# Optimization experiments

Measured on AMD Instinct MI355X. Metric: run time of the kernel, lower is better.

The kernel has to match this reference:

```python
import jax, jax.numpy as jnp
import numpy as np

NPIX = 12288
NBUCKETS = 32
IN_DIM = 32
OUT_DIM = 128
LN_EPS = 1e-5


def setup_inputs() -> dict:
    key = jax.random.key(0)
    ks = jax.random.split(key, 8)
    N = 2000000
    nbatch = 4
    obs_features = jax.random.normal(ks[0], (N, IN_DIM), dtype=jnp.float32)
    batch_idx = jax.random.randint(ks[1], (N,), 0, nbatch, dtype=jnp.int64 if jax.config.jax_enable_x64 else jnp.int32).astype(jnp.int32)
    pix = jax.random.randint(ks[2], (N,), 0, NPIX).astype(jnp.int32)
    bucket_id = jax.random.randint(ks[3], (N,), 0, NBUCKETS).astype(jnp.int32)
    proj_in = NBUCKETS * IN_DIM + NBUCKETS  # 1056
    proj_out = 2 * OUT_DIM  # 256
    W1 = jax.random.normal(ks[4], (proj_in, proj_out), dtype=jnp.float32) / np.sqrt(proj_in)
    b1 = jnp.zeros((proj_out,), dtype=jnp.float32)
    ln_g = jnp.ones((proj_out,), dtype=jnp.float32)
    ln_b = jnp.zeros((proj_out,), dtype=jnp.float32)
    W2 = jax.random.normal(ks[5], (proj_out, OUT_DIM), dtype=jnp.float32) / np.sqrt(proj_out)
    b2 = jnp.zeros((OUT_DIM,), dtype=jnp.float32)
    return {"obs_features": obs_features, "batch_idx": batch_idx, "pix": pix,
            "bucket_id": bucket_id, "nbatch": nbatch,
            "W1": W1, "b1": b1, "ln_g": ln_g, "ln_b": ln_b, "W2": W2, "b2": b2}


def reference(obs_features, batch_idx, pix, bucket_id, nbatch, W1, b1, ln_g, ln_b, W2, b2):
    # Flatten (batch, pix, bucket) coords row-major, as in scatter_mean's strides.
    flat_idx = (batch_idx.astype(jnp.int32) * (NPIX * NBUCKETS)
                + pix.astype(jnp.int32) * NBUCKETS
                + bucket_id.astype(jnp.int32))
    grid_size = nbatch * NPIX * NBUCKETS
    # scatter-mean: segment sums and counts over the flat grid
    sums = jax.ops.segment_sum(obs_features, flat_idx, num_segments=grid_size)  # (G, C)
    counts = jax.ops.segment_sum(jnp.ones((obs_features.shape[0],), obs_features.dtype),
                                 flat_idx, num_segments=grid_size)  # (G,)
    present = counts > 0
    # NaN fill for empty cells followed by nan_to_num(0) == zero fill for empty cells
    mean = jnp.where(present[:, None], sums / jnp.maximum(counts, 1.0)[:, None], 0.0)
    aggregated = mean.reshape(nbatch, NPIX, NBUCKETS * IN_DIM)
    has_obs = present.reshape(nbatch, NPIX, NBUCKETS).astype(obs_features.dtype)
    mlp_in = jnp.concatenate([aggregated, has_obs], axis=-1)  # (B, npix, proj_in)
    h = mlp_in @ W1 + b1
    mu = jnp.mean(h, axis=-1, keepdims=True)
    var = jnp.mean(jnp.square(h - mu), axis=-1, keepdims=True)
    h = (h - mu) * jax.lax.rsqrt(var + LN_EPS) * ln_g + ln_b
    h = jax.nn.silu(h)
    return h @ W2 + b2  # (B, npix, out_dim)
```

## Files before the change

kernel.cpp:

```cpp
#include <hip/hip_runtime.h>
#include <cstddef>
#include <cstdint>
#include <cmath>

#define NPIX     12288
#define NBUCKETS 32
#define IN_DIM   32
#define PROJ_IN  1056
#define PROJ_OUT 256
#define OUT_DIM  128
#define LN_EPS   1e-5f
#define NBATCH   4

#define ROWS   (NBATCH * NPIX)
#define GCELLS (ROWS * NBUCKETS)

#define BM 64
#define BK 32

#define SCAN_CHUNK 2048
#define NBLK_SCAN  (GCELLS / SCAN_CHUNK)

__global__ __launch_bounds__(256)
void flat_hist_kernel(const int* __restrict__ bidx, const int* __restrict__ pix,
                      const int* __restrict__ bucket, int* __restrict__ flat,
                      int* __restrict__ cnt, int N)
{
    int p = blockIdx.x * 256 + threadIdx.x;
    if (p >= N) return;
    int f = bidx[p] * (NPIX * NBUCKETS) + pix[p] * NBUCKETS + bucket[p];
    flat[p] = f;
    atomicAdd(&cnt[f], 1);
}

__global__ __launch_bounds__(256)
void scan_reduce_kernel(const int* __restrict__ cnt, int* __restrict__ partials)
{
    __shared__ int wsum[4];
    const int b = blockIdx.x, t = threadIdx.x;
    const int4* src = reinterpret_cast<const int4*>(cnt + (size_t)b * SCAN_CHUNK);
    int4 v0 = src[t * 2], v1 = src[t * 2 + 1];
    int s = v0.x + v0.y + v0.z + v0.w + v1.x + v1.y + v1.z + v1.w;
#pragma unroll
    for (int off = 32; off; off >>= 1) s += __shfl_xor(s, off);
    if ((t & 63) == 0) wsum[t >> 6] = s;
    __syncthreads();
    if (t == 0) partials[b] = wsum[0] + wsum[1] + wsum[2] + wsum[3];
}

__global__ void scan_mid_kernel(int* __restrict__ partials)
{
    const int t = threadIdx.x;
    int v[12]; int s = 0;
#pragma unroll
    for (int i = 0; i < 12; ++i) { v[i] = partials[t * 12 + i]; s += v[i]; }
    int inc = s;
#pragma unroll
    for (int d = 1; d < 64; d <<= 1) { int o = __shfl_up(inc, d); if (t >= d) inc += o; }
    int base = inc - s;
#pragma unroll
    for (int i = 0; i < 12; ++i) { int x = v[i]; partials[t * 12 + i] = base; base += x; }
}

__global__ __launch_bounds__(256)
void scan_write_kernel(const int* __restrict__ partials,
                       int* __restrict__ offs, int* __restrict__ cursor)
{
    __shared__ int wbase[4];
    const int b = blockIdx.x, t = threadIdx.x;
    const int lane = t & 63, w = t >> 6;
    const int4* src = reinterpret_cast<const int4*>(cursor + (size_t)b * SCAN_CHUNK);
    int4 v0 = src[t * 2], v1 = src[t * 2 + 1];
    int a[8] = { v0.x, v0.y, v0.z, v0.w, v1.x, v1.y, v1.z, v1.w };
    int s = 0;
#pragma unroll
    for (int i = 0; i < 8; ++i) s += a[i];
    int inc = s;
#pragma unroll
    for (int d = 1; d < 64; d <<= 1) { int o = __shfl_up(inc, d); if (lane >= d) inc += o; }
    if (lane == 63) wbase[w] = inc;
    __syncthreads();
    int wb = 0;
    for (int i = 0; i < w; ++i) wb += wbase[i];
    int base = partials[b] + wb + (inc - s);
    const int idx0 = b * SCAN_CHUNK + t * 8;
#pragma unroll
    for (int i = 0; i < 8; ++i) { offs[idx0 + i] = base; cursor[idx0 + i] = base; base += a[i]; }
    if (b == (int)gridDim.x - 1 && t == 255) offs[GCELLS] = base;
}

__global__ __launch_bounds__(256)
void reorder_kernel(const int* __restrict__ flat, int* __restrict__ cursor,
                    int* __restrict__ order, int N)
{
    int p = blockIdx.x * 256 + threadIdx.x;
    if (p >= N) return;
    int f = flat[p];
    int slot = atomicAdd(&cursor[f], 1);
    order[slot] = p;
}

__global__ void zero_out_kernel(float* __restrict__ out, size_t n)
{
    size_t i = (size_t)blockIdx.x * blockDim.x + threadIdx.x;
    if (i < n) out[i] = 0.f;
}

__global__ __launch_bounds__(256, 3)
void fused_mlp_kernel(const float* __restrict__ feats,
                      const int*   __restrict__ order_g,
                      const int*   __restrict__ offs_g,
                      const float* __restrict__ W1,
                      const float* __restrict__ b1,
                      const float* __restrict__ ln_g,
                      const float* __restrict__ ln_b,
                      const float* __restrict__ W2,
                      const float* __restrict__ b2,
                      float* __restrict__ out)
{
    __shared__ __align__(16) float smem[8192 + 2048 + 2052];
    float* Bs   = smem;
    float* As   = smem + 8192;
    int*   offsT = reinterpret_cast<int*>(smem + 8192 + 2048);
    float* h_s  = smem;

    const int t    = threadIdx.x;
    const int row0 = blockIdx.x * BM;
    const int tr   = t >> 5;
    const int tc   = t & 31;
    const int m0   = tr * 8;
    const int c0   = tc * 8;

    {
        const int4* s4 = reinterpret_cast<const int4*>(offs_g + (size_t)row0 * NBUCKETS);
        int4* d4 = reinterpret_cast<int4*>(offsT);
        d4[t]       = s4[t];
        d4[t + 256] = s4[t + 256];
        if (t == 0) offsT[2048] = offs_g[(size_t)row0 * NBUCKETS + 2048];
    }
    __syncthreads();

    float acc[8][8];
#pragma unroll
    for (int i = 0; i < 8; ++i)
#pragma unroll
        for (int j = 0; j < 8; ++j) acc[i][j] = 0.f;

    const int ar = t >> 3;
    const int aq = t & 7;
    const float4* feats4 = reinterpret_cast<const float4*>(feats);

    for (int s = 0; s < 33; ++s) {
        {
            const float4* src = reinterpret_cast<const float4*>(W1 + (size_t)s * BK * PROJ_OUT);
            float4* dst = reinterpret_cast<float4*>(Bs);
#pragma unroll
            for (int i = 0; i < 8; ++i) dst[t + i * 256] = src[t + i * 256];
        }
        if (s < 32) {
#pragma unroll
            for (int h = 0; h < 2; ++h) {
                const int r = ar + h * 32;
                const int cell = r * NBUCKETS + s;
                const int start = offsT[cell], end = offsT[cell + 1];
                float4 a4 = make_float4(0.f, 0.f, 0.f, 0.f);
                for (int j = start; j < end; ++j) {
                    const int idx = order_g[j];
                    const float4 v = feats4[(size_t)idx * 8 + aq];
                    a4.x += v.x; a4.y += v.y; a4.z += v.z; a4.w += v.w;
                }
                const int cnt = end - start;
                const float inv = cnt ? 1.0f / (float)cnt : 0.f;
                As[(aq * 4 + 0) * 64 + r] = a4.x * inv;
                As[(aq * 4 + 1) * 64 + r] = a4.y * inv;
                As[(aq * 4 + 2) * 64 + r] = a4.z * inv;
                As[(aq * 4 + 3) * 64 + r] = a4.w * inv;
            }
        } else {
#pragma unroll
            for (int h = 0; h < 2; ++h) {
                const int r = ar + h * 32;
#pragma unroll
                for (int i = 0; i < 4; ++i) {
                    const int kk = aq * 4 + i;
                    As[kk * 64 + r] = (offsT[r * NBUCKETS + kk + 1] > offsT[r * NBUCKETS + kk]) ? 1.f : 0.f;
                }
            }
        }
        __syncthreads();

#pragma unroll 8
        for (int kk = 0; kk < BK; ++kk) {
            float a[8], b[8];
            *reinterpret_cast<float4*>(&a[0]) = *reinterpret_cast<const float4*>(&As[kk * 64 + m0]);
            *reinterpret_cast<float4*>(&a[4]) = *reinterpret_cast<const float4*>(&As[kk * 64 + m0 + 4]);
            *reinterpret_cast<float4*>(&b[0]) = *reinterpret_cast<const float4*>(&Bs[kk * 256 + c0]);
            *reinterpret_cast<float4*>(&b[4]) = *reinterpret_cast<const float4*>(&Bs[kk * 256 + c0 + 4]);
#pragma unroll
            for (int i = 0; i < 8; ++i)
#pragma unroll
                for (int j = 0; j < 8; ++j)
                    acc[i][j] = fmaf(a[i], b[j], acc[i][j]);
        }
        __syncthreads();
    }

    float b1v[8];
    *reinterpret_cast<float4*>(&b1v[0]) = *reinterpret_cast<const float4*>(&b1[c0]);
    *reinterpret_cast<float4*>(&b1v[4]) = *reinterpret_cast<const float4*>(&b1[c0 + 4]);

    const int lane = t & 63;
    const int wv   = t >> 6;
    const float g0 = ln_g[lane], g1 = ln_g[lane + 64], g2 = ln_g[lane + 128], g3 = ln_g[lane + 192];
    const float e0 = ln_b[lane], e1 = ln_b[lane + 64], e2 = ln_b[lane + 128], e3 = ln_b[lane + 192];

    for (int half = 0; half < 2; ++half) {
        __syncthreads();
        if ((tr >> 2) == half) {
            const int mb = m0 - half * 32;
#pragma unroll
            for (int i = 0; i < 8; ++i) {
                float4 w0 = make_float4(acc[i][0] + b1v[0], acc[i][1] + b1v[1],
                                        acc[i][2] + b1v[2], acc[i][3] + b1v[3]);
                float4 w1 = make_float4(acc[i][4] + b1v[4], acc[i][5] + b1v[5],
                                        acc[i][6] + b1v[6], acc[i][7] + b1v[7]);
                *reinterpret_cast<float4*>(&h_s[(mb + i) * 256 + c0])     = w0;
                *reinterpret_cast<float4*>(&h_s[(mb + i) * 256 + c0 + 4]) = w1;
            }
        }
        __syncthreads();

        for (int r = wv; r < 32; r += 4) {
            float v0 = h_s[r * 256 + lane];
            float v1 = h_s[r * 256 + lane + 64];
            float v2 = h_s[r * 256 + lane + 128];
            float v3 = h_s[r * 256 + lane + 192];
            float sum = v0 + v1 + v2 + v3;
            float sq  = fmaf(v0, v0, fmaf(v1, v1, fmaf(v2, v2, v3 * v3)));
#pragma unroll
            for (int off = 32; off > 0; off >>= 1) {
                sum += __shfl_xor(sum, off);
                sq  += __shfl_xor(sq, off);
            }
            const float mu  = sum * (1.0f / 256.0f);
            const float var = sq * (1.0f / 256.0f) - mu * mu;
            const float rs  = rsqrtf(var + LN_EPS);
            v0 = fmaf((v0 - mu) * rs, g0, e0);
            v1 = fmaf((v1 - mu) * rs, g1, e1);
            v2 = fmaf((v2 - mu) * rs, g2, e2);
            v3 = fmaf((v3 - mu) * rs, g3, e3);
            v0 = v0 / (1.f + expf(-v0));
            v1 = v1 / (1.f + expf(-v1));
            v2 = v2 / (1.f + expf(-v2));
            v3 = v3 / (1.f + expf(-v3));
            h_s[r * 256 + lane]       = v0;
            h_s[r * 256 + lane + 64]  = v1;
            h_s[r * 256 + lane + 128] = v2;
            h_s[r * 256 + lane + 192] = v3;
        }
        __syncthreads();

        {
            const int c  = t & 127;
            const int gg = t >> 7;
            float acc2[16];
#pragma unroll
            for (int i = 0; i < 16; ++i) acc2[i] = 0.f;
            for (int k = 0; k < 256; k += 4) {
                const float wa = W2[(k + 0) * 128 + c];
                const float wb = W2[(k + 1) * 128 + c];
                const float wc = W2[(k + 2) * 128 + c];
                const float wd = W2[(k + 3) * 128 + c];
#pragma unroll
                for (int i = 0; i < 16; ++i) {
                    const float4 h4 = *reinterpret_cast<const float4*>(&h_s[(gg * 16 + i) * 256 + k]);
                    acc2[i] = fmaf(h4.x, wa, acc2[i]);
                    acc2[i] = fmaf(h4.y, wb, acc2[i]);
                    acc2[i] = fmaf(h4.z, wc, acc2[i]);
                    acc2[i] = fmaf(h4.w, wd, acc2[i]);
                }
            }
            const float bias = b2[c];
#pragma unroll
            for (int i = 0; i < 16; ++i) {
                const int m = gg * 16 + i;
                out[(size_t)(row0 + half * 32 + m) * 128 + c] = acc2[i] + bias;
            }
        }
    }
}

extern "C" void kernel_launch(void* const* d_in, const int* in_sizes, int n_in,
                              void* d_out, int out_size, void* d_ws, size_t ws_size,
                              hipStream_t stream)
{
    const float* feats  = (const float*)d_in[0];
    const int*   bidx   = (const int*)d_in[1];
    const int*   pix    = (const int*)d_in[2];
    const int*   bucket = (const int*)d_in[3];
    const float* W1   = (const float*)d_in[5];
    const float* b1   = (const float*)d_in[6];
    const float* ln_g = (const float*)d_in[7];
    const float* ln_b = (const float*)d_in[8];
    const float* W2   = (const float*)d_in[9];
    const float* b2   = (const float*)d_in[10];
    float* out = (float*)d_out;

    const int N = in_sizes[1];

    int* flat     = (int*)d_ws;
    int* order    = flat + N;
    int* cursor   = order + N;
    int* offs     = cursor + GCELLS;
    int* partials = offs + GCELLS + 1;

    const size_t ws_needed = ((size_t)2 * N + 2 * GCELLS + 1 + NBLK_SCAN) * sizeof(int);
    if (ws_size < ws_needed) {
        size_t n = (size_t)out_size;
        zero_out_kernel<<<(unsigned)((n + 255) / 256), 256, 0, stream>>>(out, n);
        return;
    }

    hipMemsetAsync(cursor, 0, (size_t)GCELLS * sizeof(int), stream);

    const int pgrid = (N + 255) / 256;
    flat_hist_kernel<<<pgrid, 256, 0, stream>>>(bidx, pix, bucket, flat, cursor, N);
    scan_reduce_kernel<<<NBLK_SCAN, 256, 0, stream>>>(cursor, partials);
    scan_mid_kernel<<<1, 64, 0, stream>>>(partials);
    scan_write_kernel<<<NBLK_SCAN, 256, 0, stream>>>(partials, offs, cursor);
    reorder_kernel<<<pgrid, 256, 0, stream>>>(flat, cursor, order, N);

    fused_mlp_kernel<<<ROWS / BM, 256, 0, stream>>>(feats, order, offs, W1, b1,
                                                    ln_g, ln_b, W2, b2, out);
}
```

Baseline: 1.049 ms.

## Move fused MLP onto bf16x3 MFMA with pre-swizzled split weights

Rewrites the fused scatter-mean MLP kernel so both GEMMs use 16x16x32 bf16 MFMA instructions. It emulates fp32 precision with hi/lo bf16 splits (three products per tile). A new kernel pre-swizzles W1 and W2 into per-lane bf16 hi/lo records each call. LayerNorm and SiLU now run directly on the accumulator registers instead of passing through shared memory. The reorder pass drops its second atomic by recording each point's rank during the histogram, at the cost of an extra N-sized rank buffer and some precision loss from the bf16 splitting.

```diff
diff --git a/kernel.cpp b/kernel.cpp
--- a/kernel.cpp
+++ b/kernel.cpp
@@ -15,22 +15,68 @@
 #define ROWS   (NBATCH * NPIX)
 #define GCELLS (ROWS * NBUCKETS)
 
-#define BM 64
-#define BK 32
-
 #define SCAN_CHUNK 2048
 #define NBLK_SCAN  (GCELLS / SCAN_CHUNK)
 
+#define W1RECS (33 * 16 * 64)
+#define W2RECS (8 * 8 * 64)
+
+typedef __attribute__((ext_vector_type(8))) short bf16x8;
+typedef __attribute__((ext_vector_type(4))) float f32x4;
+
+__device__ inline unsigned bf16_rne_bits(float v) {
+    unsigned u = __float_as_uint(v);
+    return (u + 0x7FFFu + ((u >> 16) & 1u)) >> 16;
+}
+
+__global__ __launch_bounds__(256)
+void swz_kernel(const float* __restrict__ W1, const float* __restrict__ W2,
+                bf16x8* __restrict__ w1h, bf16x8* __restrict__ w1l,
+                bf16x8* __restrict__ w2h, bf16x8* __restrict__ w2l)
+{
+    const int T = blockIdx.x * 256 + threadIdx.x;
+    if (T < W1RECS) {
+        const int l = T & 63, n0 = (T >> 6) & 15, s = T >> 10;
+        const int col  = n0 * 16 + (l & 15);
+        const int krow = s * 32 + (l >> 4) * 8;
+        bf16x8 vh, vl;
+#pragma unroll
+        for (int j = 0; j < 8; ++j) {
+            const float v = W1[(size_t)(krow + j) * PROJ_OUT + col];
+            const unsigned hb = bf16_rne_bits(v);
+            const float hf = __uint_as_float(hb << 16);
+            const unsigned lb = bf16_rne_bits(v - hf);
+            vh[j] = (short)hb; vl[j] = (short)lb;
+        }
+        w1h[T] = vh; w1l[T] = vl;
+    } else if (T < W1RECS + W2RECS) {
+        const int T2 = T - W1RECS;
+        const int l = T2 & 63, n0 = (T2 >> 6) & 7, s2 = T2 >> 9;
+        const int col  = n0 * 16 + (l & 15);
+        const int krow = s2 * 32 + (l >> 4) * 8;
+        bf16x8 vh, vl;
+#pragma unroll
+        for (int j = 0; j < 8; ++j) {
+            const float v = W2[(size_t)(krow + j) * OUT_DIM + col];
+            const unsigned hb = bf16_rne_bits(v);
+            const float hf = __uint_as_float(hb << 16);
+            const unsigned lb = bf16_rne_bits(v - hf);
+            vh[j] = (short)hb; vl[j] = (short)lb;
+        }
+        w2h[T2] = vh; w2l[T2] = vl;
+    }
+}
+
 __global__ __launch_bounds__(256)
 void flat_hist_kernel(const int* __restrict__ bidx, const int* __restrict__ pix,
                       const int* __restrict__ bucket, int* __restrict__ flat,
-                      int* __restrict__ cnt, int N)
+                      int* __restrict__ rank, int* __restrict__ cnt, int N)
 {
     int p = blockIdx.x * 256 + threadIdx.x;
     if (p >= N) return;
     int f = bidx[p] * (NPIX * NBUCKETS) + pix[p] * NBUCKETS + bucket[p];
     flat[p] = f;
-    atomicAdd(&cnt[f], 1);
+    rank[p] = atomicAdd(&cnt[f], 1);
 }
 
 __global__ __launch_bounds__(256)
@@ -63,13 +109,13 @@
 }
 
 __global__ __launch_bounds__(256)
-void scan_write_kernel(const int* __restrict__ partials,
-                       int* __restrict__ offs, int* __restrict__ cursor)
+void scan_write_kernel(const int* __restrict__ partials, const int* __restrict__ cnt,
+                       int* __restrict__ offs)
 {
     __shared__ int wbase[4];
     const int b = blockIdx.x, t = threadIdx.x;
     const int lane = t & 63, w = t >> 6;
-    const int4* src = reinterpret_cast<const int4*>(cursor + (size_t)b * SCAN_CHUNK);
+    const int4* src = reinterpret_cast<const int4*>(cnt + (size_t)b * SCAN_CHUNK);
     int4 v0 = src[t * 2], v1 = src[t * 2 + 1];
     int a[8] = { v0.x, v0.y, v0.z, v0.w, v1.x, v1.y, v1.z, v1.w };
     int s = 0;
@@ -85,19 +131,17 @@
     int base = partials[b] + wb + (inc - s);
     const int idx0 = b * SCAN_CHUNK + t * 8;
 #pragma unroll
-    for (int i = 0; i < 8; ++i) { offs[idx0 + i] = base; cursor[idx0 + i] = base; base += a[i]; }
+    for (int i = 0; i < 8; ++i) { offs[idx0 + i] = base; base += a[i]; }
     if (b == (int)gridDim.x - 1 && t == 255) offs[GCELLS] = base;
 }
 
 __global__ __launch_bounds__(256)
-void reorder_kernel(const int* __restrict__ flat, int* __restrict__ cursor,
-                    int* __restrict__ order, int N)
+void reorder_kernel(const int* __restrict__ flat, const int* __restrict__ rank,
+                    const int* __restrict__ offs, int* __restrict__ order, int N)
 {
     int p = blockIdx.x * 256 + threadIdx.x;
     if (p >= N) return;
-    int f = flat[p];
-    int slot = atomicAdd(&cursor[f], 1);
-    order[slot] = p;
+    order[offs[flat[p]] + rank[p]] = p;
 }
 
 __global__ void zero_out_kernel(float* __restrict__ out, size_t n)
@@ -107,185 +151,177 @@
 }
 
 __global__ __launch_bounds__(256, 3)
-void fused_mlp_kernel(const float* __restrict__ feats,
-                      const int*   __restrict__ order_g,
-                      const int*   __restrict__ offs_g,
-                      const float* __restrict__ W1,
-                      const float* __restrict__ b1,
-                      const float* __restrict__ ln_g,
-                      const float* __restrict__ ln_b,
-                      const float* __restrict__ W2,
-                      const float* __restrict__ b2,
-                      float* __restrict__ out)
-{
-    __shared__ __align__(16) float smem[8192 + 2048 + 2052];
-    float* Bs   = smem;
-    float* As   = smem + 8192;
-    int*   offsT = reinterpret_cast<int*>(smem + 8192 + 2048);
-    float* h_s  = smem;
-
-    const int t    = threadIdx.x;
-    const int row0 = blockIdx.x * BM;
-    const int tr   = t >> 5;
-    const int tc   = t & 31;
-    const int m0   = tr * 8;
-    const int c0   = tc * 8;
-
-    {
-        const int4* s4 = reinterpret_cast<const int4*>(offs_g + (size_t)row0 * NBUCKETS);
-        int4* d4 = reinterpret_cast<int4*>(offsT);
-        d4[t]       = s4[t];
-        d4[t + 256] = s4[t + 256];
-        if (t == 0) offsT[2048] = offs_g[(size_t)row0 * NBUCKETS + 2048];
+void fused_mlp_mfma(const float* __restrict__ feats,
+                    const int*   __restrict__ order_g,
+                    const int*   __restrict__ offs_g,
+                    const bf16x8* __restrict__ w1h, const bf16x8* __restrict__ w1l,
+                    const bf16x8* __restrict__ w2h, const bf16x8* __restrict__ w2l,
+                    const float* __restrict__ b1,   const float* __restrict__ ln_g,
+                    const float* __restrict__ ln_b, const float* __restrict__ b2,
+                    float* __restrict__ out)
+{
+    __shared__ int offsT[64 * 33];
+    __shared__ __align__(16) short hfH[4][2048];
+    __shared__ __align__(16) short hfL[4][2048];
+
+    const int t  = threadIdx.x;
+    const int w  = t >> 6;
+    const int l  = t & 63;
+    const int g  = l >> 4;
+    const int li = l & 15;
+    const int row0 = blockIdx.x * 64;
+    const int rl = w * 16 + li;
+
+    for (int i = t; i < 64 * 33; i += 256) {
+        const int r = i / 33, b = i - r * 33;
+        offsT[i] = offs_g[(size_t)row0 * 32 + r * 32 + b];
     }
     __syncthreads();
 
-    float acc[8][8];
-#pragma unroll
-    for (int i = 0; i < 8; ++i)
-#pragma unroll
-        for (int j = 0; j < 8; ++j) acc[i][j] = 0.f;
-
-    const int ar = t >> 3;
-    const int aq = t & 7;
+    f32x4 acc[16];
+#pragma unroll
+    for (int n0 = 0; n0 < 16; ++n0) acc[n0] = (f32x4){0.f, 0.f, 0.f, 0.f};
+
     const float4* feats4 = reinterpret_cast<const float4*>(feats);
 
     for (int s = 0; s < 33; ++s) {
-        {
-            const float4* src = reinterpret_cast<const float4*>(W1 + (size_t)s * BK * PROJ_OUT);
-            float4* dst = reinterpret_cast<float4*>(Bs);
-#pragma unroll
-            for (int i = 0; i < 8; ++i) dst[t + i * 256] = src[t + i * 256];
-        }
+        float m[8];
         if (s < 32) {
-#pragma unroll
-            for (int h = 0; h < 2; ++h) {
-                const int r = ar + h * 32;
-                const int cell = r * NBUCKETS + s;
-                const int start = offsT[cell], end = offsT[cell + 1];
-                float4 a4 = make_float4(0.f, 0.f, 0.f, 0.f);
-                for (int j = start; j < end; ++j) {
-                    const int idx = order_g[j];
-                    const float4 v = feats4[(size_t)idx * 8 + aq];
-                    a4.x += v.x; a4.y += v.y; a4.z += v.z; a4.w += v.w;
-                }
-                const int cnt = end - start;
-                const float inv = cnt ? 1.0f / (float)cnt : 0.f;
-                As[(aq * 4 + 0) * 64 + r] = a4.x * inv;
-                As[(aq * 4 + 1) * 64 + r] = a4.y * inv;
-                As[(aq * 4 + 2) * 64 + r] = a4.z * inv;
-                As[(aq * 4 + 3) * 64 + r] = a4.w * inv;
-            }
+            const int start = offsT[rl * 33 + s];
+            const int end   = offsT[rl * 33 + s + 1];
+            float4 a0 = make_float4(0.f, 0.f, 0.f, 0.f);
+            float4 a1 = make_float4(0.f, 0.f, 0.f, 0.f);
+            for (int j2 = start; j2 < end; ++j2) {
+                const int idx = order_g[j2];
+                const float4 p0 = feats4[(size_t)idx * 8 + g * 2];
+                const float4 p1 = feats4[(size_t)idx * 8 + g * 2 + 1];
+                a0.x += p0.x; a0.y += p0.y; a0.z += p0.z; a0.w += p0.w;
+                a1.x += p1.x; a1.y += p1.y; a1.z += p1.z; a1.w += p1.w;
+            }
+            const float inv = (end > start) ? 1.f / (float)(end - start) : 0.f;
+            m[0] = a0.x * inv; m[1] = a0.y * inv; m[2] = a0.z * inv; m[3] = a0.w * inv;
+            m[4] = a1.x * inv; m[5] = a1.y * inv; m[6] = a1.z * inv; m[7] = a1.w * inv;
         } else {
 #pragma unroll
-            for (int h = 0; h < 2; ++h) {
-                const int r = ar + h * 32;
-#pragma unroll
-                for (int i = 0; i < 4; ++i) {
-                    const int kk = aq * 4 + i;
-                    As[kk * 64 + r] = (offsT[r * NBUCKETS + kk + 1] > offsT[r * NBUCKETS + kk]) ? 1.f : 0.f;
-                }
-            }
-        }
-        __syncthreads();
-
-#pragma unroll 8
-        for (int kk = 0; kk < BK; ++kk) {
-            float a[8], b[8];
-            *reinterpret_cast<float4*>(&a[0]) = *reinterpret_cast<const float4*>(&As[kk * 64 + m0]);
-            *reinterpret_cast<float4*>(&a[4]) = *reinterpret_cast<const float4*>(&As[kk * 64 + m0 + 4]);
-            *reinterpret_cast<float4*>(&b[0]) = *reinterpret_cast<const float4*>(&Bs[kk * 256 + c0]);
-            *reinterpret_cast<float4*>(&b[4]) = *reinterpret_cast<const float4*>(&Bs[kk * 256 + c0 + 4]);
-#pragma unroll
-            for (int i = 0; i < 8; ++i)
-#pragma unroll
-                for (int j = 0; j < 8; ++j)
-                    acc[i][j] = fmaf(a[i], b[j], acc[i][j]);
-        }
-        __syncthreads();
-    }
-
-    float b1v[8];
-    *reinterpret_cast<float4*>(&b1v[0]) = *reinterpret_cast<const float4*>(&b1[c0]);
-    *reinterpret_cast<float4*>(&b1v[4]) = *reinterpret_cast<const float4*>(&b1[c0 + 4]);
-
-    const int lane = t & 63;
-    const int wv   = t >> 6;
-    const float g0 = ln_g[lane], g1 = ln_g[lane + 64], g2 = ln_g[lane + 128], g3 = ln_g[lane + 192];
-    const float e0 = ln_b[lane], e1 = ln_b[lane + 64], e2 = ln_b[lane + 128], e3 = ln_b[lane + 192];
-
-    for (int half = 0; half < 2; ++half) {
-        __syncthreads();
-        if ((tr >> 2) == half) {
-            const int mb = m0 - half * 32;
-#pragma unroll
-            for (int i = 0; i < 8; ++i) {
-                float4 w0 = make_float4(acc[i][0] + b1v[0], acc[i][1] + b1v[1],
-                                        acc[i][2] + b1v[2], acc[i][3] + b1v[3]);
-                float4 w1 = make_float4(acc[i][4] + b1v[4], acc[i][5] + b1v[5],
-                                        acc[i][6] + b1v[6], acc[i][7] + b1v[7]);
-                *reinterpret_cast<float4*>(&h_s[(mb + i) * 256 + c0])     = w0;
-                *reinterpret_cast<float4*>(&h_s[(mb + i) * 256 + c0 + 4]) = w1;
-            }
-        }
-        __syncthreads();
-
-        for (int r = wv; r < 32; r += 4) {
-            float v0 = h_s[r * 256 + lane];
-            float v1 = h_s[r * 256 + lane + 64];
-            float v2 = h_s[r * 256 + lane + 128];
-            float v3 = h_s[r * 256 + lane + 192];
-            float sum = v0 + v1 + v2 + v3;
-            float sq  = fmaf(v0, v0, fmaf(v1, v1, fmaf(v2, v2, v3 * v3)));
-#pragma unroll
-            for (int off = 32; off > 0; off >>= 1) {
-                sum += __shfl_xor(sum, off);
-                sq  += __shfl_xor(sq, off);
-            }
-            const float mu  = sum * (1.0f / 256.0f);
-            const float var = sq * (1.0f / 256.0f) - mu * mu;
-            const float rs  = rsqrtf(var + LN_EPS);
-            v0 = fmaf((v0 - mu) * rs, g0, e0);
-            v1 = fmaf((v1 - mu) * rs, g1, e1);
-            v2 = fmaf((v2 - mu) * rs, g2, e2);
-            v3 = fmaf((v3 - mu) * rs, g3, e3);
-            v0 = v0 / (1.f + expf(-v0));
-            v1 = v1 / (1.f + expf(-v1));
-            v2 = v2 / (1.f + expf(-v2));
-            v3 = v3 / (1.f + expf(-v3));
-            h_s[r * 256 + lane]       = v0;
-            h_s[r * 256 + lane + 64]  = v1;
-            h_s[r * 256 + lane + 128] = v2;
-            h_s[r * 256 + lane + 192] = v3;
-        }
-        __syncthreads();
-
-        {
-            const int c  = t & 127;
-            const int gg = t >> 7;
-            float acc2[16];
-#pragma unroll
-            for (int i = 0; i < 16; ++i) acc2[i] = 0.f;
-            for (int k = 0; k < 256; k += 4) {
-                const float wa = W2[(k + 0) * 128 + c];
-                const float wb = W2[(k + 1) * 128 + c];
-                const float wc = W2[(k + 2) * 128 + c];
-                const float wd = W2[(k + 3) * 128 + c];
-#pragma unroll
-                for (int i = 0; i < 16; ++i) {
-                    const float4 h4 = *reinterpret_cast<const float4*>(&h_s[(gg * 16 + i) * 256 + k]);
-                    acc2[i] = fmaf(h4.x, wa, acc2[i]);
-                    acc2[i] = fmaf(h4.y, wb, acc2[i]);
-                    acc2[i] = fmaf(h4.z, wc, acc2[i]);
-                    acc2[i] = fmaf(h4.w, wd, acc2[i]);
-                }
-            }
-            const float bias = b2[c];
-#pragma unroll
-            for (int i = 0; i < 16; ++i) {
-                const int m = gg * 16 + i;
-                out[(size_t)(row0 + half * 32 + m) * 128 + c] = acc2[i] + bias;
-            }
+            for (int j = 0; j < 8; ++j) {
+                const int b = g * 8 + j;
+                m[j] = (offsT[rl * 33 + b + 1] > offsT[rl * 33 + b]) ? 1.f : 0.f;
+            }
+        }
+        bf16x8 ah, al;
+#pragma unroll
+        for (int j = 0; j < 8; ++j) {
+            const unsigned u = __float_as_uint(m[j]);
+            ah[j] = (short)(u >> 16);
+            const float rlo = m[j] - __uint_as_float(u & 0xFFFF0000u);
+            al[j] = (short)(__float_as_uint(rlo) >> 16);
+        }
+        const int base = (s * 16) * 64 + l;
+        if (s < 32) {
+#pragma unroll 4
+            for (int n0 = 0; n0 < 16; ++n0) {
+                const bf16x8 bh = w1h[base + n0 * 64];
+                const bf16x8 bl = w1l[base + n0 * 64];
+                acc[n0] = __builtin_amdgcn_mfma_f32_16x16x32_bf16(ah, bh, acc[n0], 0, 0, 0);
+                acc[n0] = __builtin_amdgcn_mfma_f32_16x16x32_bf16(ah, bl, acc[n0], 0, 0, 0);
+                acc[n0] = __builtin_amdgcn_mfma_f32_16x16x32_bf16(al, bh, acc[n0], 0, 0, 0);
+            }
+        } else {
+#pragma unroll 4
+            for (int n0 = 0; n0 < 16; ++n0) {
+                const bf16x8 bh = w1h[base + n0 * 64];
+                const bf16x8 bl = w1l[base + n0 * 64];
+                acc[n0] = __builtin_amdgcn_mfma_f32_16x16x32_bf16(ah, bh, acc[n0], 0, 0, 0);
+                acc[n0] = __builtin_amdgcn_mfma_f32_16x16x32_bf16(ah, bl, acc[n0], 0, 0, 0);
+            }
+        }
+    }
+
+    float sum[4] = {0.f, 0.f, 0.f, 0.f}, sq[4] = {0.f, 0.f, 0.f, 0.f};
+#pragma unroll
+    for (int n0 = 0; n0 < 16; ++n0) {
+        const float bb = b1[n0 * 16 + li];
+#pragma unroll
+        for (int r = 0; r < 4; ++r) {
+            const float v = acc[n0][r] + bb;
+            acc[n0][r] = v;
+            sum[r] += v;
+            sq[r] = fmaf(v, v, sq[r]);
+        }
+    }
+#pragma unroll
+    for (int off = 1; off < 16; off <<= 1) {
+#pragma unroll
+        for (int r = 0; r < 4; ++r) {
+            sum[r] += __shfl_xor(sum[r], off);
+            sq[r]  += __shfl_xor(sq[r], off);
+        }
+    }
+    float mu[4], rs[4];
+#pragma unroll
+    for (int r = 0; r < 4; ++r) {
+        mu[r] = sum[r] * (1.f / 256.f);
+        const float var = sq[r] * (1.f / 256.f) - mu[r] * mu[r];
+        rs[r] = rsqrtf(var + LN_EPS);
+    }
+#pragma unroll
+    for (int n0 = 0; n0 < 16; ++n0) {
+        const float gg = ln_g[n0 * 16 + li];
+        const float eb = ln_b[n0 * 16 + li];
+#pragma unroll
+        for (int r = 0; r < 4; ++r) {
+            float v = fmaf((acc[n0][r] - mu[r]) * rs[r], gg, eb);
+            v = v / (1.f + __expf(-v));
+            acc[n0][r] = v;
+        }
+    }
+
+    f32x4 acc2[8];
+#pragma unroll
+    for (int n0 = 0; n0 < 8; ++n0) acc2[n0] = (f32x4){0.f, 0.f, 0.f, 0.f};
+
+    for (int p = 0; p < 2; ++p) {
+#pragma unroll
+        for (int q = 0; q < 8; ++q) {
+            const int n0 = p * 8 + q;
+            const int c = n0 * 16 + li;
+            const int s2l = (c >> 5) & 3;
+            const int kk = c & 31;
+            const int wbase = s2l * 512 + (kk >> 3) * 128 + (kk & 7);
+#pragma unroll
+            for (int r = 0; r < 4; ++r) {
+                const float v = acc[n0][r];
+                const unsigned u = __float_as_uint(v);
+                const short hi = (short)(u >> 16);
+                const float rlo = v - __uint_as_float(u & 0xFFFF0000u);
+                const short lo = (short)(__float_as_uint(rlo) >> 16);
+                const int a = wbase + (g * 4 + r) * 8;
+                hfH[w][a] = hi;
+                hfL[w][a] = lo;
+            }
+        }
+#pragma unroll
+        for (int s2l = 0; s2l < 4; ++s2l) {
+            const bf16x8 a2h = *reinterpret_cast<const bf16x8*>(&hfH[w][(s2l * 64 + l) * 8]);
+            const bf16x8 a2l = *reinterpret_cast<const bf16x8*>(&hfL[w][(s2l * 64 + l) * 8]);
+            const int b2base = ((p * 4 + s2l) * 8) * 64 + l;
+#pragma unroll 4
+            for (int n0 = 0; n0 < 8; ++n0) {
+                const bf16x8 bh = w2h[b2base + n0 * 64];
+                const bf16x8 bl = w2l[b2base + n0 * 64];
+                acc2[n0] = __builtin_amdgcn_mfma_f32_16x16x32_bf16(a2h, bh, acc2[n0], 0, 0, 0);
+                acc2[n0] = __builtin_amdgcn_mfma_f32_16x16x32_bf16(a2h, bl, acc2[n0], 0, 0, 0);
+                acc2[n0] = __builtin_amdgcn_mfma_f32_16x16x32_bf16(a2l, bh, acc2[n0], 0, 0, 0);
+            }
+        }
+    }
+
+#pragma unroll
+    for (int n0 = 0; n0 < 8; ++n0) {
+        const float bb = b2[n0 * 16 + li];
+#pragma unroll
+        for (int r = 0; r < 4; ++r) {
+            out[(size_t)(row0 + w * 16 + g * 4 + r) * OUT_DIM + n0 * 16 + li] = acc2[n0][r] + bb;
         }
     }
 }
@@ -309,27 +345,37 @@
     const int N = in_sizes[1];
 
     int* flat     = (int*)d_ws;
-    int* order    = flat + N;
-    int* cursor   = order + N;
-    int* offs     = cursor + GCELLS;
+    int* rank     = flat + N;
+    int* order    = rank + N;
+    int* cnt      = order + N;
+    int* offs     = cnt + GCELLS;
     int* partials = offs + GCELLS + 1;
-
-    const size_t ws_needed = ((size_t)2 * N + 2 * GCELLS + 1 + NBLK_SCAN) * sizeof(int);
+    const size_t int_bytes = ((size_t)3 * N + 2 * GCELLS + 1 + NBLK_SCAN) * sizeof(int);
+    const size_t swz_off = (int_bytes + 15) & ~(size_t)15;
+    bf16x8* w1h = (bf16x8*)((char*)d_ws + swz_off);
+    bf16x8* w1l = w1h + W1RECS;
+    bf16x8* w2h = w1l + W1RECS;
+    bf16x8* w2l = w2h + W2RECS;
+    const size_t ws_needed = swz_off + (size_t)(2 * W1RECS + 2 * W2RECS) * 16;
+
     if (ws_size < ws_needed) {
         size_t n = (size_t)out_size;
         zero_out_kernel<<<(unsigned)((n + 255) / 256), 256, 0, stream>>>(out, n);
         return;
     }
 
-    hipMemsetAsync(cursor, 0, (size_t)GCELLS * sizeof(int), stream);
+    hipMemsetAsync(cnt, 0, (size_t)GCELLS * sizeof(int), stream);
+
+    swz_kernel<<<(W1RECS + W2RECS + 255) / 256, 256, 0, stream>>>(W1, W2, w1h, w1l, w2h, w2l);
 
     const int pgrid = (N + 255) / 256;
-    flat_hist_kernel<<<pgrid, 256, 0, stream>>>(bidx, pix, bucket, flat, cursor, N);
-    scan_reduce_kernel<<<NBLK_SCAN, 256, 0, stream>>>(cursor, partials);
+    flat_hist_kernel<<<pgrid, 256, 0, stream>>>(bidx, pix, bucket, flat, rank, cnt, N);
+    scan_reduce_kernel<<<NBLK_SCAN, 256, 0, stream>>>(cnt, partials);
     scan_mid_kernel<<<1, 64, 0, stream>>>(partials);
-    scan_write_kernel<<<NBLK_SCAN, 256, 0, stream>>>(partials, offs, cursor);
-    reorder_kernel<<<pgrid, 256, 0, stream>>>(flat, cursor, order, N);
-
-    fused_mlp_kernel<<<ROWS / BM, 256, 0, stream>>>(feats, order, offs, W1, b1,
-                                                    ln_g, ln_b, W2, b2, out);
-}
+    scan_write_kernel<<<NBLK_SCAN, 256, 0, stream>>>(partials, cnt, offs);
+    reorder_kernel<<<pgrid, 256, 0, stream>>>(flat, rank, offs, order, N);
+
+    fused_mlp_mfma<<<ROWS / 64, 256, 0, stream>>>(feats, order, offs,
+                                                  w1h, w1l, w2h, w2l,
+                                                  b1, ln_g, ln_b, b2, out);
+}
```

Measured after the change: 1.317 ms. 1.26x slower.
